# Kernel optimization log

Hardware: AMD Instinct MI355X
Metric: run time of the kernel (lower is better)

Reference implementation:

```python
import jax, jax.numpy as jnp
import numpy as np

EPS = 1e-5

def layernorm(x, g, b):
    mu = jnp.mean(x, axis=-1, keepdims=True)
    var = jnp.mean(jnp.square(x - mu), axis=-1, keepdims=True)
    return (x - mu) * jax.lax.rsqrt(var + EPS) * g + b

def setup_inputs() -> dict:
    key = jax.random.key(0)
    ks = jax.random.split(key, 12)
    B, T, C, H = 4, 2048, 1024, 8
    Dh = C // H          # 128
    Dff = 4 * C          # 4096
    s = 0.02
    return {
        "x":     jax.random.normal(ks[0], (B, T, C), jnp.float32),
        "wq":    jax.random.normal(ks[1], (H, C, Dh), jnp.float32) * s,
        "wk":    jax.random.normal(ks[2], (H, C, Dh), jnp.float32) * s,
        "wv":    jax.random.normal(ks[3], (H, C, Dh), jnp.float32) * s,
        "w1":    jax.random.normal(ks[4], (C, Dff), jnp.float32) * s,
        "b1":    jnp.zeros((Dff,), jnp.float32),
        "w2":    jax.random.normal(ks[5], (Dff, C), jnp.float32) * s,
        "b2":    jnp.zeros((C,), jnp.float32),
        "ln1_g": jnp.ones((C,), jnp.float32),
        "ln1_b": jnp.zeros((C,), jnp.float32),
        "ln2_g": jnp.ones((C,), jnp.float32),
        "ln2_b": jnp.zeros((C,), jnp.float32),
    }

def reference(x, wq, wk, wv, w1, b1, w2, b2, ln1_g, ln1_b, ln2_g, ln2_b):
    B, T, C = x.shape
    H, _, Dh = wq.shape
    # --- multi-head self-attention (pre-LN) ---
    h = layernorm(x, ln1_g, ln1_b)
    q = jnp.einsum("btc,hcd->bhtd", h, wq)
    k = jnp.einsum("btc,hcd->bhtd", h, wk)
    v = jnp.einsum("btc,hcd->bhtd", h, wv)
    # NOTE: original multiplies by sqrt(head_size) (not divide) -- kept faithful
    scores = jnp.einsum("bhtd,bhsd->bhts", q, k) * (Dh ** 0.5)
    attn = jax.nn.softmax(scores, axis=-1)
    # dropout(p=0.2) treated as identity (eval mode)
    o = jnp.einsum("bhts,bhsd->bhtd", attn, v)
    # concat heads along last dim: head h fills contiguous slice
    o = o.transpose(0, 2, 1, 3).reshape(B, T, H * Dh)
    x = x + o  # no output projection in original module
    # --- feed-forward (pre-LN) ---
    h2 = layernorm(x, ln2_g, ln2_b)
    ff = jax.nn.relu(h2 @ w1 + b1) @ w2 + b2
    return x + ff
```

## Files before the change

### kernel.cpp

```cpp
#include <hip/hip_runtime.h>
#include <hip/hip_bf16.h>
#include <math.h>

#define B_   4
#define T_   2048
#define C_   1024
#define H_   8
#define DH   128
#define DFF  4096
#define M_   (B_*T_)

typedef __attribute__((ext_vector_type(8))) short bf16x8;
typedef __attribute__((ext_vector_type(4))) float f32x4;

#define SC2 16.32223094f

__device__ __forceinline__ unsigned short f2bf(float x) {
  union { float f; unsigned u; } v; v.f = x;
  return (unsigned short)((v.u + 0x7fffu + ((v.u >> 16) & 1u)) >> 16);
}
__device__ __forceinline__ float bf2f(unsigned short h) {
  union { unsigned u; float f; } v; v.u = ((unsigned)h) << 16; return v.f;
}

__device__ __forceinline__ f32x4 mfma_bf16(bf16x8 a, bf16x8 b, f32x4 c) {
  return __builtin_amdgcn_mfma_f32_16x16x32_bf16(a, b, c, 0, 0, 0);
}

__device__ __forceinline__ void gll16(const void* g, void* l) {
  __builtin_amdgcn_global_load_lds((const __attribute__((address_space(1))) void*)g,
                                   (__attribute__((address_space(3))) void*)l,
                                   16, 0, 0);
}

__global__ __launch_bounds__(256) void ln_kernel(const float* __restrict__ in,
                                                 const float* __restrict__ g,
                                                 const float* __restrict__ bb,
                                                 unsigned short* __restrict__ h_hi,
                                                 unsigned short* __restrict__ h_lo) {
  __shared__ float red[8];
  const int row = blockIdx.x;
  const int tid = threadIdx.x;
  const float* p = in + (size_t)row * C_;
  const float4 xv = *(const float4*)(p + (tid << 2));
  float s  = xv.x + xv.y + xv.z + xv.w;
  float sq = xv.x*xv.x + xv.y*xv.y + xv.z*xv.z + xv.w*xv.w;
  #pragma unroll
  for (int off = 32; off > 0; off >>= 1) {
    s  += __shfl_xor(s, off);
    sq += __shfl_xor(sq, off);
  }
  if ((tid & 63) == 0) { red[(tid >> 6) * 2] = s; red[(tid >> 6) * 2 + 1] = sq; }
  __syncthreads();
  s  = red[0] + red[2] + red[4] + red[6];
  sq = red[1] + red[3] + red[5] + red[7];
  const float mu  = s * (1.0f / C_);
  const float var = sq * (1.0f / C_) - mu * mu;
  const float rs  = rsqrtf(var + 1e-5f);
  const float4 gv = *(const float4*)(g  + (tid << 2));
  const float4 bv = *(const float4*)(bb + (tid << 2));
  float ov[4];
  ov[0] = (xv.x - mu) * rs * gv.x + bv.x;
  ov[1] = (xv.y - mu) * rs * gv.y + bv.y;
  ov[2] = (xv.z - mu) * rs * gv.z + bv.z;
  ov[3] = (xv.w - mu) * rs * gv.w + bv.w;
  ushort4 hv, lv;
  unsigned short* hp = (unsigned short*)&hv;
  unsigned short* lp = (unsigned short*)&lv;
  #pragma unroll
  for (int j = 0; j < 4; ++j) {
    hp[j] = f2bf(ov[j]);
    lp[j] = f2bf(ov[j] - bf2f(hp[j]));
  }
  *(ushort4*)(h_hi + (size_t)row * C_ + (tid << 2)) = hv;
  *(ushort4*)(h_lo + (size_t)row * C_ + (tid << 2)) = lv;
}

__global__ __launch_bounds__(256) void cvt_t_kernel(const float* __restrict__ in,
                                                    unsigned short* __restrict__ out,
                                                    int R, int CC) {
  __shared__ float tile[32][33];
  const int r0 = blockIdx.y << 5, c0 = blockIdx.x << 5;
  const int tr = threadIdx.x >> 3, tc4 = (threadIdx.x & 7) << 2;
  const float4 vv = *(const float4*)(in + (size_t)(r0 + tr) * CC + c0 + tc4);
  tile[tr][tc4+0] = vv.x; tile[tr][tc4+1] = vv.y;
  tile[tr][tc4+2] = vv.z; tile[tr][tc4+3] = vv.w;
  __syncthreads();
  ushort4 o;
  o.x = f2bf(tile[tc4+0][tr]); o.y = f2bf(tile[tc4+1][tr]);
  o.z = f2bf(tile[tc4+2][tr]); o.w = f2bf(tile[tc4+3][tr]);
  *(ushort4*)(out + (size_t)(c0 + tr) * R + r0 + tc4) = o;
}

__global__ __launch_bounds__(256) void cvt_qkv_kernel(const float* __restrict__ wq,
                                                      const float* __restrict__ wk,
                                                      const float* __restrict__ wv,
                                                      unsigned short* __restrict__ wt_hi,
                                                      unsigned short* __restrict__ wt_lo) {
  const int z = blockIdx.z;
  const int which = z >> 3, head = z & 7;
  const float* in = (which == 0 ? wq : (which == 1 ? wk : wv)) + (size_t)head * C_ * DH;
  unsigned short* oh = wt_hi + (size_t)z * DH * C_;
  unsigned short* ol = wt_lo + (size_t)z * DH * C_;
  __shared__ float tile[32][33];
  const int r0 = blockIdx.y << 5, c0 = blockIdx.x << 5;
  const int tr = threadIdx.x >> 3, tc4 = (threadIdx.x & 7) << 2;
  const float4 vv = *(const float4*)(in + (size_t)(r0 + tr) * DH + c0 + tc4);
  tile[tr][tc4+0] = vv.x; tile[tr][tc4+1] = vv.y;
  tile[tr][tc4+2] = vv.z; tile[tr][tc4+3] = vv.w;
  __syncthreads();
  ushort4 hv, lv;
  unsigned short* hp = (unsigned short*)&hv;
  unsigned short* lp = (unsigned short*)&lv;
  #pragma unroll
  for (int j = 0; j < 4; ++j) {
    const float val = tile[tc4+j][tr];
    hp[j] = f2bf(val);
    lp[j] = f2bf(val - bf2f(hp[j]));
  }
  *(ushort4*)(oh + (size_t)(c0 + tr) * C_ + r0 + tc4) = hv;
  *(ushort4*)(ol + (size_t)(c0 + tr) * C_ + r0 + tc4) = lv;
}

template<int TERMS>
__device__ __forceinline__ void gemm128_mfma(
    const unsigned short* __restrict__ Ah, const unsigned short* __restrict__ Al,
    int lda,
    const unsigned short* __restrict__ Bh, const unsigned short* __restrict__ Bl,
    int ldb, int K, f32x4 (&acc)[4][4],
    unsigned short* AhS, unsigned short* AlS,
    unsigned short* BhS, unsigned short* BlS) {
  const int tid  = threadIdx.x;
  const int w    = tid >> 6;
  const int lane = tid & 63;
  const int l15  = lane & 15, quad = lane >> 4;
  const int srow = lane >> 2, skc = (lane & 3) << 3;
  const int wm = w & 1, wn = w >> 1;

  for (int k0 = 0; k0 < K; k0 += 32) {
    __syncthreads();
    #pragma unroll
    for (int i = 0; i < 2; ++i) {
      const int seg  = w * 2 + i;
      const int r    = seg * 16 + srow;
      const int lofs = seg * 512 + lane * 8;
      gll16(Ah + (size_t)r * lda + k0 + skc, AhS + lofs);
      gll16(Bh + (size_t)r * ldb + k0 + skc, BhS + lofs);
      if (TERMS == 3) {
        gll16(Al + (size_t)r * lda + k0 + skc, AlS + lofs);
        gll16(Bl + (size_t)r * ldb + k0 + skc, BlS + lofs);
      }
    }
    __syncthreads();
    bf16x8 aH[4], bH[4], aL[4], bL[4];
    #pragma unroll
    for (int t = 0; t < 4; ++t) {
      aH[t] = *(const bf16x8*)&AhS[(wm * 64 + t * 16 + l15) * 32 + quad * 8];
      bH[t] = *(const bf16x8*)&BhS[(wn * 64 + t * 16 + l15) * 32 + quad * 8];
      if (TERMS == 3) {
        aL[t] = *(const bf16x8*)&AlS[(wm * 64 + t * 16 + l15) * 32 + quad * 8];
        bL[t] = *(const bf16x8*)&BlS[(wn * 64 + t * 16 + l15) * 32 + quad * 8];
      }
    }
    #pragma unroll
    for (int rt = 0; rt < 4; ++rt)
      #pragma unroll
      for (int ct = 0; ct < 4; ++ct) {
        if (TERMS == 3) {
          acc[rt][ct] = mfma_bf16(aL[rt], bH[ct], acc[rt][ct]);
          acc[rt][ct] = mfma_bf16(aH[rt], bL[ct], acc[rt][ct]);
        }
        acc[rt][ct] = mfma_bf16(aH[rt], bH[ct], acc[rt][ct]);
      }
  }
}

__global__ __launch_bounds__(256) void qkm_kernel(const unsigned short* __restrict__ h_hi,
                                                  const unsigned short* __restrict__ h_lo,
                                                  const unsigned short* __restrict__ wt_hi,
                                                  const unsigned short* __restrict__ wt_lo,
                                                  unsigned short* __restrict__ q_hi,
                                                  unsigned short* __restrict__ q_lo,
                                                  unsigned short* __restrict__ k_hi,
                                                  unsigned short* __restrict__ k_lo) {
  __shared__ __align__(16) unsigned short AhS[4096], AlS[4096];
  __shared__ __align__(16) unsigned short BhS[4096], BlS[4096];
  const int m0 = blockIdx.x << 7;
  const int z  = blockIdx.y;
  const int which = z >> 3, head = z & 7;
  f32x4 acc[4][4];
  #pragma unroll
  for (int i = 0; i < 4; ++i)
    #pragma unroll
    for (int j = 0; j < 4; ++j)
      #pragma unroll
      for (int r = 0; r < 4; ++r) acc[i][j][r] = 0.f;
  gemm128_mfma<3>(h_hi + (size_t)m0 * C_, h_lo + (size_t)m0 * C_, C_,
                  wt_hi + (size_t)z * DH * C_, wt_lo + (size_t)z * DH * C_, C_,
                  C_, acc, AhS, AlS, BhS, BlS);
  const int lane = threadIdx.x & 63, w = threadIdx.x >> 6;
  const int l15 = lane & 15, quad = lane >> 4;
  const int wm = w & 1, wn = w >> 1;
  const int bh = (m0 >> 11) * H_ + head;
  const int tbase = (m0 & (T_ - 1)) + wm * 64 + quad * 4;
  if (which == 0) {
    #pragma unroll
    for (int rt = 0; rt < 4; ++rt)
      #pragma unroll
      for (int ct = 0; ct < 4; ++ct) {
        const int d = wn * 64 + ct * 16 + l15;
        #pragma unroll
        for (int r = 0; r < 4; ++r) {
          const int t = tbase + rt * 16 + r;
          const float val = acc[rt][ct][r] * SC2;
          const unsigned short hb = f2bf(val);
          const size_t idx = ((size_t)bh * T_ + t) * DH + d;
          q_hi[idx] = hb;
          q_lo[idx] = f2bf(val - bf2f(hb));
        }
      }
  } else {
    #pragma unroll
    for (int rt = 0; rt < 4; ++rt)
      #pragma unroll
      for (int ct = 0; ct < 4; ++ct) {
        const int d = wn * 64 + ct * 16 + l15;
        #pragma unroll
        for (int r = 0; r < 4; ++r) {
          const int t = tbase + rt * 16 + r;
          const float val = acc[rt][ct][r];
          const unsigned short hb = f2bf(val);
          const size_t idx = (((size_t)bh * 64 + (t >> 5)) * 4 + (d >> 5)) * 1024
                           + (size_t)(t & 31) * 32 + (d & 31);
          k_hi[idx] = hb;
          k_lo[idx] = f2bf(val - bf2f(hb));
        }
      }
  }
}

__global__ __launch_bounds__(256) void vm_kernel(const unsigned short* __restrict__ h_hi,
                                                 const unsigned short* __restrict__ wv_hi,
                                                 unsigned short* __restrict__ vimg) {
  __shared__ __align__(16) unsigned short AhS[4096], BhS[4096];
  const int m0 = blockIdx.x << 7;
  const int head = blockIdx.y;
  f32x4 acc[4][4];
  #pragma unroll
  for (int i = 0; i < 4; ++i)
    #pragma unroll
    for (int j = 0; j < 4; ++j)
      #pragma unroll
      for (int r = 0; r < 4; ++r) acc[i][j][r] = 0.f;
  gemm128_mfma<1>(h_hi + (size_t)m0 * C_, nullptr, C_,
                  wv_hi + (size_t)(16 + head) * DH * C_, nullptr, C_,
                  C_, acc, AhS, nullptr, BhS, nullptr);
  const int lane = threadIdx.x & 63, w = threadIdx.x >> 6;
  const int l15 = lane & 15, quad = lane >> 4;
  const int wm = w & 1, wn = w >> 1;
  const int bh = (m0 >> 11) * H_ + head;
  #pragma unroll
  for (int rt = 0; rt < 4; ++rt)
    #pragma unroll
    for (int ct = 0; ct < 4; ++ct) {
      const int d  = wn * 64 + ct * 16 + l15;
      const int t0 = (m0 & (T_ - 1)) + wm * 64 + rt * 16 + quad * 4;
      ushort4 pk;
      pk.x = f2bf(acc[rt][ct][0]); pk.y = f2bf(acc[rt][ct][1]);
      pk.z = f2bf(acc[rt][ct][2]); pk.w = f2bf(acc[rt][ct][3]);
      *(ushort4*)&vimg[(((size_t)bh * 64 + (t0 >> 5)) * 128 + d) * 32 + (t0 & 31)] = pk;
    }
}

__global__ __launch_bounds__(256) void ff1_kernel(const unsigned short* __restrict__ h2,
                                                  const unsigned short* __restrict__ w1t,
                                                  const float* __restrict__ b1,
                                                  unsigned short* __restrict__ ff1) {
  __shared__ __align__(16) unsigned short AhS[4096], BhS[4096];
  const int n0 = blockIdx.x << 7;
  const int m0 = blockIdx.y << 7;
  f32x4 acc[4][4];
  #pragma unroll
  for (int i = 0; i < 4; ++i)
    #pragma unroll
    for (int j = 0; j < 4; ++j)
      #pragma unroll
      for (int r = 0; r < 4; ++r) acc[i][j][r] = 0.f;
  gemm128_mfma<1>(h2 + (size_t)m0 * C_, nullptr, C_,
                  w1t + (size_t)n0 * C_, nullptr, C_,
                  C_, acc, AhS, nullptr, BhS, nullptr);
  const int lane = threadIdx.x & 63, w = threadIdx.x >> 6;
  const int l15 = lane & 15, quad = lane >> 4;
  const int wm = w & 1, wn = w >> 1;
  #pragma unroll
  for (int rt = 0; rt < 4; ++rt)
    #pragma unroll
    for (int ct = 0; ct < 4; ++ct) {
      const int n = n0 + wn * 64 + ct * 16 + l15;
      const float bias = b1[n];
      #pragma unroll
      for (int r = 0; r < 4; ++r) {
        const int m = m0 + wm * 64 + rt * 16 + quad * 4 + r;
        ff1[(size_t)m * DFF + n] = f2bf(fmaxf(acc[rt][ct][r] + bias, 0.f));
      }
    }
}

__global__ __launch_bounds__(256) void ff2_kernel(const unsigned short* __restrict__ ff1,
                                                  const unsigned short* __restrict__ w2t,
                                                  const float* __restrict__ b2,
                                                  const float* __restrict__ xo,
                                                  float* __restrict__ out) {
  __shared__ __align__(16) unsigned short AhS[4096], BhS[4096];
  const int n0 = blockIdx.x << 7;
  const int m0 = blockIdx.y << 7;
  f32x4 acc[4][4];
  #pragma unroll
  for (int i = 0; i < 4; ++i)
    #pragma unroll
    for (int j = 0; j < 4; ++j)
      #pragma unroll
      for (int r = 0; r < 4; ++r) acc[i][j][r] = 0.f;
  gemm128_mfma<1>(ff1 + (size_t)m0 * DFF, nullptr, DFF,
                  w2t + (size_t)n0 * DFF, nullptr, DFF,
                  DFF, acc, AhS, nullptr, BhS, nullptr);
  const int lane = threadIdx.x & 63, w = threadIdx.x >> 6;
  const int l15 = lane & 15, quad = lane >> 4;
  const int wm = w & 1, wn = w >> 1;
  #pragma unroll
  for (int rt = 0; rt < 4; ++rt)
    #pragma unroll
    for (int ct = 0; ct < 4; ++ct) {
      const int n = n0 + wn * 64 + ct * 16 + l15;
      const float bias = b2[n];
      #pragma unroll
      for (int r = 0; r < 4; ++r) {
        const int m = m0 + wm * 64 + rt * 16 + quad * 4 + r;
        out[(size_t)m * C_ + n] = acc[rt][ct][r] + bias + xo[(size_t)m * C_ + n];
      }
    }
}

#define BQ 128

__global__ __launch_bounds__(256, 2) void attn_kernel(
    const unsigned short* __restrict__ q_hi, const unsigned short* __restrict__ q_lo,
    const unsigned short* __restrict__ k_hi, const unsigned short* __restrict__ k_lo,
    const unsigned short* __restrict__ vimg,
    const float* __restrict__ x, float* __restrict__ xo) {
  __shared__ __align__(16) unsigned short KhS[4096];
  __shared__ __align__(16) unsigned short KlS[4096];
  __shared__ __align__(16) unsigned short VtS[4096];
  __shared__ __align__(16) unsigned short PS [4096];

  const int bh  = blockIdx.y;
  const int qt0 = blockIdx.x * BQ;
  const int tid  = threadIdx.x;
  const int w    = tid >> 6;
  const int lane = tid & 63;
  const int l15  = lane & 15;
  const int quad = lane >> 4;

  bf16x8 Qh[2][4], Ql[2][4];
  #pragma unroll
  for (int rt = 0; rt < 2; ++rt) {
    const int row = qt0 + w * 32 + rt * 16 + l15;
    #pragma unroll
    for (int kc = 0; kc < 4; ++kc) {
      const size_t off = ((size_t)bh * T_ + row) * DH + kc * 32 + quad * 8;
      Qh[rt][kc] = *(const bf16x8*)(q_hi + off);
      Ql[rt][kc] = *(const bf16x8*)(q_lo + off);
    }
  }

  f32x4 O[2][8];
  #pragma unroll
  for (int rt = 0; rt < 2; ++rt)
    #pragma unroll
    for (int n = 0; n < 8; ++n)
      #pragma unroll
      for (int r = 0; r < 4; ++r) O[rt][n][r] = 0.f;
  float m_i[2][4], l_i[2][4];
  #pragma unroll
  for (int rt = 0; rt < 2; ++rt)
    #pragma unroll
    for (int r = 0; r < 4; ++r) { m_i[rt][r] = -1e30f; l_i[rt][r] = 0.f; }

  for (int kt = 0; kt < T_ / 32; ++kt) {
    const size_t tb = ((size_t)bh * 64 + kt) * 4096;
    __syncthreads();
    #pragma unroll
    for (int i = 0; i < 2; ++i) {
      const int ofs = (w * 2 + i) * 512 + lane * 8;
      gll16(k_hi + tb + ofs, KhS + ofs);
      gll16(k_lo + tb + ofs, KlS + ofs);
      gll16(vimg + tb + ofs, VtS + ofs);
    }
    __syncthreads();

    f32x4 S[2][2];
    #pragma unroll
    for (int rt = 0; rt < 2; ++rt)
      #pragma unroll
      for (int ct = 0; ct < 2; ++ct)
        #pragma unroll
        for (int r = 0; r < 4; ++r) S[rt][ct][r] = 0.f;
    #pragma unroll
    for (int kc = 0; kc < 4; ++kc) {
      const int o = kc * 1024 + quad * 8;
      const bf16x8 bh0 = *(const bf16x8*)&KhS[o + l15 * 32];
      const bf16x8 bh1 = *(const bf16x8*)&KhS[o + (16 + l15) * 32];
      const bf16x8 bl0 = *(const bf16x8*)&KlS[o + l15 * 32];
      const bf16x8 bl1 = *(const bf16x8*)&KlS[o + (16 + l15) * 32];
      #pragma unroll
      for (int rt = 0; rt < 2; ++rt) {
        S[rt][0] = mfma_bf16(Ql[rt][kc], bh0, S[rt][0]);
        S[rt][0] = mfma_bf16(Qh[rt][kc], bl0, S[rt][0]);
        S[rt][0] = mfma_bf16(Qh[rt][kc], bh0, S[rt][0]);
        S[rt][1] = mfma_bf16(Ql[rt][kc], bh1, S[rt][1]);
        S[rt][1] = mfma_bf16(Qh[rt][kc], bl1, S[rt][1]);
        S[rt][1] = mfma_bf16(Qh[rt][kc], bh1, S[rt][1]);
      }
    }

    #pragma unroll
    for (int rt = 0; rt < 2; ++rt) {
      #pragma unroll
      for (int r = 0; r < 4; ++r) {
        const float s0 = S[rt][0][r];
        const float s1 = S[rt][1][r];
        float mx = fmaxf(s0, s1);
        #pragma unroll
        for (int msk = 1; msk < 16; msk <<= 1) mx = fmaxf(mx, __shfl_xor(mx, msk));
        const float m_new = fmaxf(m_i[rt][r], mx);
        const float alpha = exp2f(m_i[rt][r] - m_new);
        m_i[rt][r] = m_new;
        const float p0 = exp2f(s0 - m_new);
        const float p1 = exp2f(s1 - m_new);
        float rs = p0 + p1;
        #pragma unroll
        for (int msk = 1; msk < 16; msk <<= 1) rs += __shfl_xor(rs, msk);
        l_i[rt][r] = l_i[rt][r] * alpha + rs;
        #pragma unroll
        for (int n = 0; n < 8; ++n) O[rt][n][r] *= alpha;
        const int prow = w * 32 + rt * 16 + quad * 4 + r;
        PS[prow * 32 + l15]      = (unsigned short)(__float_as_uint(p0) >> 16);
        PS[prow * 32 + 16 + l15] = (unsigned short)(__float_as_uint(p1) >> 16);
      }
    }
    __syncthreads();

    bf16x8 aP[2];
    #pragma unroll
    for (int rt = 0; rt < 2; ++rt)
      aP[rt] = *(const bf16x8*)&PS[(w * 32 + rt * 16 + l15) * 32 + quad * 8];
    #pragma unroll
    for (int n = 0; n < 8; ++n) {
      const bf16x8 bv = *(const bf16x8*)&VtS[(n * 16 + l15) * 32 + quad * 8];
      O[0][n] = mfma_bf16(aP[0], bv, O[0][n]);
      O[1][n] = mfma_bf16(aP[1], bv, O[1][n]);
    }
  }

  const int b = bh >> 3, hh = bh & 7;
  #pragma unroll
  for (int rt = 0; rt < 2; ++rt) {
    #pragma unroll
    for (int r = 0; r < 4; ++r) {
      const float inv_l = 1.0f / l_i[rt][r];
      const int t = qt0 + w * 32 + rt * 16 + quad * 4 + r;
      const size_t xrow = ((size_t)(b * T_ + t)) * C_ + (size_t)hh * DH;
      #pragma unroll
      for (int n = 0; n < 8; ++n) {
        const int d = n * 16 + l15;
        xo[xrow + d] = x[xrow + d] + O[rt][n][r] * inv_l;
      }
    }
  }
}

extern "C" void kernel_launch(void* const* d_in, const int* in_sizes, int n_in,
                              void* d_out, int out_size, void* d_ws, size_t ws_size,
                              hipStream_t stream) {
  (void)in_sizes; (void)n_in; (void)out_size; (void)ws_size;
  const float* x     = (const float*)d_in[0];
  const float* wq    = (const float*)d_in[1];
  const float* wk    = (const float*)d_in[2];
  const float* wv    = (const float*)d_in[3];
  const float* w1    = (const float*)d_in[4];
  const float* b1    = (const float*)d_in[5];
  const float* w2    = (const float*)d_in[6];
  const float* b2    = (const float*)d_in[7];
  const float* ln1_g = (const float*)d_in[8];
  const float* ln1_b = (const float*)d_in[9];
  const float* ln2_g = (const float*)d_in[10];
  const float* ln2_b = (const float*)d_in[11];
  float* out = (float*)d_out;

  char* W = (char*)d_ws;
  float* xo = (float*)(W);
  unsigned short* q_hi  = (unsigned short*)(W + (32u  << 20));
  unsigned short* q_lo  = (unsigned short*)(W + (48u  << 20));
  unsigned short* k_hi  = (unsigned short*)(W + (64u  << 20));
  unsigned short* k_lo  = (unsigned short*)(W + (80u  << 20));
  unsigned short* vimg  = (unsigned short*)(W + (96u  << 20));
  unsigned short* ff1   = (unsigned short*)(W + (32u  << 20));
  unsigned short* h_hi  = (unsigned short*)(W + (112u << 20));
  unsigned short* h_lo  = (unsigned short*)(W + (128u << 20));
  unsigned short* w1t   = (unsigned short*)(W + (144u << 20));
  unsigned short* w2t   = (unsigned short*)(W + (152u << 20));
  unsigned short* wt_hi = (unsigned short*)(W + (160u << 20));
  unsigned short* wt_lo = (unsigned short*)(W + (166u << 20));

  cvt_t_kernel<<<dim3(DFF / 32, C_ / 32), 256, 0, stream>>>(w1, w1t, C_, DFF);
  cvt_t_kernel<<<dim3(C_ / 32, DFF / 32), 256, 0, stream>>>(w2, w2t, DFF, C_);
  cvt_qkv_kernel<<<dim3(DH / 32, C_ / 32, 24), 256, 0, stream>>>(wq, wk, wv, wt_hi, wt_lo);
  ln_kernel<<<M_, 256, 0, stream>>>(x, ln1_g, ln1_b, h_hi, h_lo);
  qkm_kernel<<<dim3(M_ / 128, 16), 256, 0, stream>>>(h_hi, h_lo, wt_hi, wt_lo,
                                                     q_hi, q_lo, k_hi, k_lo);
  vm_kernel<<<dim3(M_ / 128, H_), 256, 0, stream>>>(h_hi, wt_hi, vimg);
  attn_kernel<<<dim3(T_ / BQ, B_ * H_), 256, 0, stream>>>(q_hi, q_lo, k_hi, k_lo,
                                                          vimg, x, xo);
  ln_kernel<<<M_, 256, 0, stream>>>(xo, ln2_g, ln2_b, h_hi, h_lo);
  ff1_kernel<<<dim3(DFF / 128, M_ / 128), 256, 0, stream>>>(h_hi, w1t, b1, ff1);
  ff2_kernel<<<dim3(C_ / 128, M_ / 128), 256, 0, stream>>>(ff1, w2t, b2, xo, out);
}
```

Before: 715.5 us.

## Restructure attention loop: 64-key tiles, transposed S, lazy rescale, swizzled P

The attention kernel now processes 64 keys per iteration instead of 32 and computes S transposed (K as the A operand), so each lane holds a full query row's scores. Row max and sum need only two cross-lane shuffles, which replaces the 4-step reductions done per register. Online-softmax rescaling is skipped unless the max grows by more than a threshold (8 in log2 units). P is written packed into a XOR-swizzled LDS layout to avoid bank conflicts, and s_setprio is raised around the MFMA sections. The removed barrier between P store and P load appears safe because each wave reads only its own rows, but LDS use doubles, which may hurt occupancy.

```diff
diff --git a/kernel.cpp b/kernel.cpp
--- a/kernel.cpp
+++ b/kernel.cpp
@@ -12,6 +12,7 @@
 
 typedef __attribute__((ext_vector_type(8))) short bf16x8;
 typedef __attribute__((ext_vector_type(4))) float f32x4;
+typedef __attribute__((ext_vector_type(2))) unsigned int u32x2;
 
 #define SC2 16.32223094f
 
@@ -348,10 +349,10 @@
     const unsigned short* __restrict__ k_hi, const unsigned short* __restrict__ k_lo,
     const unsigned short* __restrict__ vimg,
     const float* __restrict__ x, float* __restrict__ xo) {
-  __shared__ __align__(16) unsigned short KhS[4096];
-  __shared__ __align__(16) unsigned short KlS[4096];
-  __shared__ __align__(16) unsigned short VtS[4096];
-  __shared__ __align__(16) unsigned short PS [4096];
+  __shared__ __align__(16) unsigned short KhS[8192];
+  __shared__ __align__(16) unsigned short KlS[8192];
+  __shared__ __align__(16) unsigned short VtS[8192];
+  __shared__ __align__(16) unsigned short PS [8192];
 
   const int bh  = blockIdx.y;
   const int qt0 = blockIdx.x * BQ;
@@ -360,6 +361,7 @@
   const int lane = tid & 63;
   const int l15  = lane & 15;
   const int quad = lane >> 4;
+  const int srcbase = quad * 20;
 
   bf16x8 Qh[2][4], Ql[2][4];
   #pragma unroll
@@ -380,86 +382,116 @@
     for (int n = 0; n < 8; ++n)
       #pragma unroll
       for (int r = 0; r < 4; ++r) O[rt][n][r] = 0.f;
-  float m_i[2][4], l_i[2][4];
-  #pragma unroll
-  for (int rt = 0; rt < 2; ++rt)
-    #pragma unroll
-    for (int r = 0; r < 4; ++r) { m_i[rt][r] = -1e30f; l_i[rt][r] = 0.f; }
-
-  for (int kt = 0; kt < T_ / 32; ++kt) {
-    const size_t tb = ((size_t)bh * 64 + kt) * 4096;
+  float m_cur[2] = { -1e30f, -1e30f };
+  float l_cur[2] = { 0.f, 0.f };
+
+  for (int kt = 0; kt < T_ / 64; ++kt) {
+    const size_t tb = ((size_t)bh * 64 + kt * 2) * 4096;
     __syncthreads();
     #pragma unroll
-    for (int i = 0; i < 2; ++i) {
-      const int ofs = (w * 2 + i) * 512 + lane * 8;
+    for (int i = 0; i < 4; ++i) {
+      const int ofs = (w * 4 + i) * 512 + lane * 8;
       gll16(k_hi + tb + ofs, KhS + ofs);
       gll16(k_lo + tb + ofs, KlS + ofs);
       gll16(vimg + tb + ofs, VtS + ofs);
     }
     __syncthreads();
 
-    f32x4 S[2][2];
-    #pragma unroll
-    for (int rt = 0; rt < 2; ++rt)
-      #pragma unroll
-      for (int ct = 0; ct < 2; ++ct)
+    f32x4 S[4][2];
+    #pragma unroll
+    for (int ct = 0; ct < 4; ++ct)
+      #pragma unroll
+      for (int rt = 0; rt < 2; ++rt)
         #pragma unroll
-        for (int r = 0; r < 4; ++r) S[rt][ct][r] = 0.f;
+        for (int r = 0; r < 4; ++r) S[ct][rt][r] = 0.f;
+    __builtin_amdgcn_s_setprio(1);
     #pragma unroll
     for (int kc = 0; kc < 4; ++kc) {
-      const int o = kc * 1024 + quad * 8;
-      const bf16x8 bh0 = *(const bf16x8*)&KhS[o + l15 * 32];
-      const bf16x8 bh1 = *(const bf16x8*)&KhS[o + (16 + l15) * 32];
-      const bf16x8 bl0 = *(const bf16x8*)&KlS[o + l15 * 32];
-      const bf16x8 bl1 = *(const bf16x8*)&KlS[o + (16 + l15) * 32];
+      #pragma unroll
+      for (int ct = 0; ct < 4; ++ct) {
+        const int o = (ct >> 1) * 4096 + kc * 1024 + (((ct & 1) << 4) + l15) * 32 + quad * 8;
+        const bf16x8 kh = *(const bf16x8*)&KhS[o];
+        const bf16x8 kl = *(const bf16x8*)&KlS[o];
+        #pragma unroll
+        for (int rt = 0; rt < 2; ++rt) {
+          S[ct][rt] = mfma_bf16(kl, Qh[rt][kc], S[ct][rt]);
+          S[ct][rt] = mfma_bf16(kh, Ql[rt][kc], S[ct][rt]);
+          S[ct][rt] = mfma_bf16(kh, Qh[rt][kc], S[ct][rt]);
+        }
+      }
+    }
+    __builtin_amdgcn_s_setprio(0);
+
+    float mx[2];
+    #pragma unroll
+    for (int rt = 0; rt < 2; ++rt) {
+      const float c0 = fmaxf(fmaxf(S[0][rt][0], S[0][rt][1]), fmaxf(S[0][rt][2], S[0][rt][3]));
+      const float c1 = fmaxf(fmaxf(S[1][rt][0], S[1][rt][1]), fmaxf(S[1][rt][2], S[1][rt][3]));
+      const float c2 = fmaxf(fmaxf(S[2][rt][0], S[2][rt][1]), fmaxf(S[2][rt][2], S[2][rt][3]));
+      const float c3 = fmaxf(fmaxf(S[3][rt][0], S[3][rt][1]), fmaxf(S[3][rt][2], S[3][rt][3]));
+      float m0 = fmaxf(fmaxf(c0, c1), fmaxf(c2, c3));
+      m0 = fmaxf(m0, __shfl_xor(m0, 16));
+      m0 = fmaxf(m0, __shfl_xor(m0, 32));
+      mx[rt] = m0;
+    }
+
+    const int need = (mx[0] > m_cur[0] + 8.f) || (mx[1] > m_cur[1] + 8.f);
+    if (__any(need)) {
       #pragma unroll
       for (int rt = 0; rt < 2; ++rt) {
-        S[rt][0] = mfma_bf16(Ql[rt][kc], bh0, S[rt][0]);
-        S[rt][0] = mfma_bf16(Qh[rt][kc], bl0, S[rt][0]);
-        S[rt][0] = mfma_bf16(Qh[rt][kc], bh0, S[rt][0]);
-        S[rt][1] = mfma_bf16(Ql[rt][kc], bh1, S[rt][1]);
-        S[rt][1] = mfma_bf16(Qh[rt][kc], bl1, S[rt][1]);
-        S[rt][1] = mfma_bf16(Qh[rt][kc], bh1, S[rt][1]);
+        const float mn = fmaxf(m_cur[rt], mx[rt]);
+        const float al = exp2f(m_cur[rt] - mn);
+        m_cur[rt] = mn;
+        l_cur[rt] *= al;
+        #pragma unroll
+        for (int r = 0; r < 4; ++r) {
+          const float ar = __shfl(al, srcbase + r);
+          #pragma unroll
+          for (int n = 0; n < 8; ++n) O[rt][n][r] *= ar;
+        }
       }
     }
 
     #pragma unroll
     for (int rt = 0; rt < 2; ++rt) {
-      #pragma unroll
-      for (int r = 0; r < 4; ++r) {
-        const float s0 = S[rt][0][r];
-        const float s1 = S[rt][1][r];
-        float mx = fmaxf(s0, s1);
-        #pragma unroll
-        for (int msk = 1; msk < 16; msk <<= 1) mx = fmaxf(mx, __shfl_xor(mx, msk));
-        const float m_new = fmaxf(m_i[rt][r], mx);
-        const float alpha = exp2f(m_i[rt][r] - m_new);
-        m_i[rt][r] = m_new;
-        const float p0 = exp2f(s0 - m_new);
-        const float p1 = exp2f(s1 - m_new);
-        float rs = p0 + p1;
-        #pragma unroll
-        for (int msk = 1; msk < 16; msk <<= 1) rs += __shfl_xor(rs, msk);
-        l_i[rt][r] = l_i[rt][r] * alpha + rs;
-        #pragma unroll
-        for (int n = 0; n < 8; ++n) O[rt][n][r] *= alpha;
-        const int prow = w * 32 + rt * 16 + quad * 4 + r;
-        PS[prow * 32 + l15]      = (unsigned short)(__float_as_uint(p0) >> 16);
-        PS[prow * 32 + 16 + l15] = (unsigned short)(__float_as_uint(p1) >> 16);
-      }
-    }
-    __syncthreads();
-
-    bf16x8 aP[2];
-    #pragma unroll
-    for (int rt = 0; rt < 2; ++rt)
-      aP[rt] = *(const bf16x8*)&PS[(w * 32 + rt * 16 + l15) * 32 + quad * 8];
-    #pragma unroll
-    for (int n = 0; n < 8; ++n) {
-      const bf16x8 bv = *(const bf16x8*)&VtS[(n * 16 + l15) * 32 + quad * 8];
-      O[0][n] = mfma_bf16(aP[0], bv, O[0][n]);
-      O[1][n] = mfma_bf16(aP[1], bv, O[1][n]);
-    }
+      const int rowb = (w * 32 + rt * 16 + l15) * 128;
+      float rs = 0.f;
+      #pragma unroll
+      for (int ct = 0; ct < 4; ++ct) {
+        const float p0 = exp2f(S[ct][rt][0] - m_cur[rt]);
+        const float p1 = exp2f(S[ct][rt][1] - m_cur[rt]);
+        const float p2 = exp2f(S[ct][rt][2] - m_cur[rt]);
+        const float p3 = exp2f(S[ct][rt][3] - m_cur[rt]);
+        rs += (p0 + p1) + (p2 + p3);
+        u32x2 uu;
+        uu.x = (__float_as_uint(p1) & 0xffff0000u) | (__float_as_uint(p0) >> 16);
+        uu.y = (__float_as_uint(p3) & 0xffff0000u) | (__float_as_uint(p2) >> 16);
+        const int slot = (ct * 2 + (quad >> 1)) ^ (l15 & 7);
+        *(u32x2*)((char*)PS + rowb + (slot << 4) + ((quad & 1) << 3)) = uu;
+      }
+      rs += __shfl_xor(rs, 16);
+      rs += __shfl_xor(rs, 32);
+      l_cur[rt] += rs;
+    }
+
+    __builtin_amdgcn_s_setprio(1);
+    #pragma unroll
+    for (int kc = 0; kc < 2; ++kc) {
+      bf16x8 aP[2];
+      #pragma unroll
+      for (int rt = 0; rt < 2; ++rt) {
+        const int rowb = (w * 32 + rt * 16 + l15) * 128;
+        const int slot = (kc * 4 + quad) ^ (l15 & 7);
+        aP[rt] = *(const bf16x8*)((const char*)PS + rowb + (slot << 4));
+      }
+      #pragma unroll
+      for (int n = 0; n < 8; ++n) {
+        const bf16x8 bv = *(const bf16x8*)&VtS[kc * 4096 + (n * 16 + l15) * 32 + quad * 8];
+        O[0][n] = mfma_bf16(aP[0], bv, O[0][n]);
+        O[1][n] = mfma_bf16(aP[1], bv, O[1][n]);
+      }
+    }
+    __builtin_amdgcn_s_setprio(0);
   }
 
   const int b = bh >> 3, hh = bh & 7;
@@ -467,7 +499,8 @@
   for (int rt = 0; rt < 2; ++rt) {
     #pragma unroll
     for (int r = 0; r < 4; ++r) {
-      const float inv_l = 1.0f / l_i[rt][r];
+      const float lr = __shfl(l_cur[rt], srcbase + r);
+      const float inv_l = 1.0f / lr;
       const int t = qt0 + w * 32 + rt * 16 + quad * 4 + r;
       const size_t xrow = ((size_t)(b * T_ + t)) * C_ + (size_t)hh * DH;
       #pragma unroll
```

New measurement: 616.5 us. 1.16x faster.
